# Performance work log

Hardware: AMD Instinct MI355X
Metric: run time of the kernel (lower is better)

Reference implementation:

```python
import jax, jax.numpy as jnp
import numpy as np

EMBED_DIM = 1024
NUM_HEADS = 16
HEAD_DIM = EMBED_DIM // NUM_HEADS
VOCAB = 5          # languages
BOTTLENECK = 800
SCALING = HEAD_DIM ** -0.5


def setup_inputs() -> dict:
    key = jax.random.key(0)
    ks = jax.random.split(key, 16)
    T, B, D = 2048, 2, EMBED_DIM
    s = 0.02
    return {
        "query": jax.random.normal(ks[0], (T, B, D), jnp.float32),
        "key": jax.random.normal(ks[1], (T, B, D), jnp.float32),
        "value": jax.random.normal(ks[2], (T, B, D), jnp.float32),
        "wq": jax.random.normal(ks[3], (D, D), jnp.float32) * s,
        "bq": jnp.zeros((D,), jnp.float32),
        "wk": jax.random.normal(ks[4], (D, D), jnp.float32) * s,
        "bk": jnp.zeros((D,), jnp.float32),
        "wv": jax.random.normal(ks[5], (D, D), jnp.float32) * s,
        "bv": jnp.zeros((D,), jnp.float32),
        "wo": jax.random.normal(ks[6], (D, D), jnp.float32) * s,
        "bo": jnp.zeros((D,), jnp.float32),
        "wte": jax.random.normal(ks[7], (VOCAB, D), jnp.float32) * s,
        "ct_w1": jax.random.normal(ks[8], (VOCAB, BOTTLENECK, D), jnp.float32) * s,
        "ct_b1": jnp.zeros((VOCAB, BOTTLENECK), jnp.float32),
        "ct_w2": jax.random.normal(ks[9], (VOCAB, 2 * D, BOTTLENECK), jnp.float32) * s,
        "ct_b2": jnp.zeros((VOCAB, 2 * D), jnp.float32),
        "language_id": jax.random.randint(ks[10], (B,), 0, VOCAB, jnp.int32),
    }


def _prefix_kv(language_id, wte, ct_w1, ct_b1, ct_w2, ct_b2):
    # PrefixTuningLangEmbLangspec: embed lang id, run all 5 bottleneck MLPs,
    # select per-sample MLP output via one-hot weighting, split into K/V.
    B = language_id.shape[0]
    emb = wte[language_id]                                  # [B, D]
    h = jnp.tanh(jnp.einsum("bd,chd->cbh", emb, ct_w1) + ct_b1[:, None, :])  # [5,B,800]
    kv = jnp.einsum("cbh,cdh->cbd", h, ct_w2) + ct_b2[:, None, :]            # [5,B,2D]
    w = jax.nn.one_hot(language_id, VOCAB, dtype=kv.dtype)  # [B,5]
    kv_sel = jnp.einsum("bc,cbd->bd", w, kv)                # [B,2D]
    # view(b,1,2,nh,hd): first D -> keys, second D -> values
    pk = kv_sel[:, :EMBED_DIM].reshape(B, NUM_HEADS, 1, HEAD_DIM)
    pv = kv_sel[:, EMBED_DIM:].reshape(B, NUM_HEADS, 1, HEAD_DIM)
    return pk, pv


def reference(query, key, value, wq, bq, wk, bk, wv, bv, wo, bo,
              wte, ct_w1, ct_b1, ct_w2, ct_b2, language_id):
    T, B, D = query.shape
    pk, pv = _prefix_kv(language_id, wte, ct_w1, ct_b1, ct_w2, ct_b2)  # [B,H,1,hd]

    # separate Q/K/V projections (Linear: x @ W^T + b)
    q = (jnp.einsum("tbd,ed->tbe", query, wq) + bq) * SCALING
    k = jnp.einsum("tbd,ed->tbe", key, wk) + bk
    v = jnp.einsum("tbd,ed->tbe", value, wv) + bv

    # [T,B,D] -> [B,H,T,hd]
    def split_heads(x):
        return x.reshape(T, B, NUM_HEADS, HEAD_DIM).transpose(1, 2, 0, 3)

    qh = split_heads(q)
    kh = jnp.concatenate([pk, split_heads(k)], axis=2)  # [B,H,T+1,hd]
    vh = jnp.concatenate([pv, split_heads(v)], axis=2)

    scores = jnp.einsum("bhqd,bhkd->bhqk", qh, kh)      # [B,H,T,T+1]
    attn = jax.nn.softmax(scores, axis=-1)
    ctx = jnp.einsum("bhqk,bhkd->bhqd", attn, vh)       # [B,H,T,hd]

    ctx = ctx.transpose(2, 0, 1, 3).reshape(T, B, D)    # back to [T,B,D]
    out = jnp.einsum("tbd,ed->tbe", ctx, wo) + bo
    return out
```

## Files before the change

kernel.cpp:

```cpp
#include <hip/hip_runtime.h>
#include <stdint.h>

#define T_SEQ 2048
#define BATCH 2
#define DIM   1024
#define NH    16
#define HD    64
#define TKP   2112

typedef _Float16 v8h __attribute__((ext_vector_type(8)));
typedef _Float16 v4h __attribute__((ext_vector_type(4)));
typedef __fp16   pkh2 __attribute__((ext_vector_type(2)));
typedef float    f32x4 __attribute__((ext_vector_type(4)));
typedef float    f32x16 __attribute__((ext_vector_type(16)));

__device__ __forceinline__ void gload16(const _Float16* g, _Float16* l) {
  __builtin_amdgcn_global_load_lds(
      (__attribute__((address_space(1))) unsigned int*)g,
      (__attribute__((address_space(3))) unsigned int*)l, 16, 0, 0);
}

__global__ void cvt_all(const float4* __restrict__ s0, const float4* __restrict__ s1,
                        const float4* __restrict__ s2, const float4* __restrict__ s3,
                        const float4* __restrict__ s4, const float4* __restrict__ s5,
                        const float4* __restrict__ s6,
                        v4h* __restrict__ d0, v4h* __restrict__ d1, v4h* __restrict__ d2,
                        v4h* __restrict__ d3, v4h* __restrict__ d4, v4h* __restrict__ d5,
                        v4h* __restrict__ d6) {
  const int NTB4 = 1048576, DD4 = 262144;
  int i = blockIdx.x * 256 + threadIdx.x;
  const float4* s; v4h* d; int off;
  if (i < 3 * NTB4) {
    int t = i / NTB4; off = i - t * NTB4;
    s = t == 0 ? s0 : t == 1 ? s1 : s2;
    d = t == 0 ? d0 : t == 1 ? d1 : d2;
  } else {
    int j = i - 3 * NTB4;
    int t = j / DD4; off = j - t * DD4;
    s = t == 0 ? s3 : t == 1 ? s4 : t == 2 ? s5 : s6;
    d = t == 0 ? d3 : t == 1 ? d4 : t == 2 ? d5 : d6;
  }
  float4 v = s[off];
  v4h o = { (_Float16)v.x, (_Float16)v.y, (_Float16)v.z, (_Float16)v.w };
  d[off] = o;
}

__global__ void prefix_pad_k(const float* __restrict__ wte, const float* __restrict__ w1,
                             const float* __restrict__ b1, const int* __restrict__ lang,
                             float* __restrict__ hbuf,
                             _Float16* __restrict__ kb, _Float16* __restrict__ vb) {
  if (blockIdx.x >= 400) {
    int bh = blockIdx.x - 400;
    v8h z = {};
    _Float16* kp = kb + ((size_t)bh * TKP + 2048) * 64;
    for (int i = threadIdx.x; i < 512; i += 256) *(v8h*)&kp[i * 8] = z;
    for (int i = threadIdx.x; i < 512; i += 256) {
      int c = i >> 3, seg = i & 7;
      *(v8h*)&vb[((size_t)bh * 64 + c) * TKP + 2048 + seg * 8] = z;
    }
    return;
  }
  int wid = blockIdx.x * 4 + (threadIdx.x >> 6);
  int lane = threadIdx.x & 63;
  int b = wid / 800, j = wid - b * 800;
  int c = lang[b];
  const float* wr = w1 + ((size_t)c * 800 + j) * 1024;
  const float* em = wte + (size_t)c * 1024;
  float s = 0.f;
  for (int d = lane; d < 1024; d += 64) s += wr[d] * em[d];
  for (int off = 32; off > 0; off >>= 1) s += __shfl_down(s, off, 64);
  if (lane == 0) hbuf[wid] = tanhf(s + b1[c * 800 + j]);
}

__global__ void prefix_kv_k(const float* __restrict__ w2, const float* __restrict__ b2,
                            const float* __restrict__ hbuf, const int* __restrict__ lang,
                            _Float16* __restrict__ kb, _Float16* __restrict__ vb) {
  int wid = blockIdx.x * 4 + (threadIdx.x >> 6);
  int lane = threadIdx.x & 63;
  int b = wid >> 11, e = wid & 2047;
  int c = lang[b];
  const float* wr = w2 + ((size_t)c * 2048 + e) * 800;
  const float* hb = hbuf + b * 800;
  float s = 0.f;
  for (int j = lane; j < 800; j += 64) s += wr[j] * hb[j];
  for (int off = 32; off > 0; off >>= 1) s += __shfl_down(s, off, 64);
  if (lane == 0) {
    float val = s + b2[c * 2048 + e];
    if (e < 1024) {
      int h = e >> 6, hd = e & 63;
      kb[((size_t)(b * 16 + h) * TKP + 2048) * 64 + hd] = (_Float16)val;
    } else {
      int d = e - 1024;
      int h = d >> 6, hd = d & 63;
      vb[((size_t)(b * 16 + h) * 64 + hd) * TKP + 2048] = (_Float16)val;
    }
  }
}

__global__ __launch_bounds__(256) void gemm_bt_k(
    const _Float16* __restrict__ A0, const _Float16* __restrict__ A1, const _Float16* __restrict__ A2,
    const _Float16* __restrict__ W0, const _Float16* __restrict__ W1, const _Float16* __restrict__ W2,
    const float* __restrict__ bs0, const float* __restrict__ bs1, const float* __restrict__ bs2,
    _Float16* __restrict__ qb, _Float16* __restrict__ kb, _Float16* __restrict__ vb,
    float* __restrict__ fout, int mode_base)
{
  __shared__ __align__(16) _Float16 smem[2][128 * 64 * 2];
  const int mode = mode_base + blockIdx.z;
  const _Float16* A = (mode == 1) ? A1 : (mode == 2) ? A2 : A0;
  const _Float16* W = (mode == 1) ? W1 : (mode == 2) ? W2 : W0;
  const float* bias = (mode == 1) ? bs1 : (mode == 2) ? bs2 : bs0;
  const int tid = threadIdx.x, w = tid >> 6, lane = tid & 63;
  const int quad = lane >> 4, l15 = lane & 15;
  const int r0 = blockIdx.x * 128, c0 = blockIdx.y * 128;
  const int wm = w >> 1, wn = w & 1;
  const int srow = lane >> 3, sseg = lane & 7;
  const int sw_seg = sseg ^ srow;
  const int rsw = l15 & 7;
  f32x4 acc[4][4] = {};

  auto stage = [&](int k0, int p) {
    _Float16* As = smem[p];
    _Float16* Bs = smem[p] + 8192;
#pragma unroll
    for (int i = 0; i < 4; ++i) {
      int rowb = w * 32 + i * 8;
      gload16(A + (size_t)(r0 + rowb + srow) * 1024 + k0 + sw_seg * 8, &As[rowb * 64]);
      gload16(W + (size_t)(c0 + rowb + srow) * 1024 + k0 + sw_seg * 8, &Bs[rowb * 64]);
    }
  };

  stage(0, 0);
  for (int t = 0; t < 16; ++t) {
    if (t < 15) {
      stage((t + 1) << 6, (t + 1) & 1);
      asm volatile("s_waitcnt vmcnt(8)" ::: "memory");
    } else {
      asm volatile("s_waitcnt vmcnt(0)" ::: "memory");
    }
    __builtin_amdgcn_s_barrier();
    __builtin_amdgcn_sched_barrier(0);
    const _Float16* As = smem[t & 1];
    const _Float16* Bs = smem[t & 1] + 8192;
#pragma unroll
    for (int ks = 0; ks < 2; ++ks) {
      v8h af[4], bfr[4];
#pragma unroll
      for (int mt = 0; mt < 4; ++mt)
        af[mt] = *(const v8h*)&As[(wm * 64 + mt * 16 + l15) * 64 + (((ks * 4 + quad) ^ rsw) * 8)];
#pragma unroll
      for (int nt = 0; nt < 4; ++nt)
        bfr[nt] = *(const v8h*)&Bs[(wn * 64 + nt * 16 + l15) * 64 + (((ks * 4 + quad) ^ rsw) * 8)];
#pragma unroll
      for (int mt = 0; mt < 4; ++mt)
#pragma unroll
        for (int nt = 0; nt < 4; ++nt)
          acc[mt][nt] = __builtin_amdgcn_mfma_f32_16x16x32_f16(af[mt], bfr[nt], acc[mt][nt], 0, 0, 0);
    }
    __builtin_amdgcn_sched_barrier(0);
    __builtin_amdgcn_s_barrier();
  }
  if (mode == 3) {
    for (int nt = 0; nt < 4; ++nt) {
      int e = c0 + wn * 64 + nt * 16 + l15;
      float be = bias[e];
      for (int mt = 0; mt < 4; ++mt) {
        int rb = r0 + wm * 64 + mt * 16 + quad * 4;
        for (int reg = 0; reg < 4; ++reg)
          fout[(size_t)(rb + reg) * 1024 + e] = acc[mt][nt][reg] + be;
      }
    }
    return;
  }
  _Float16* st = &smem[0][0] + w * 4096;
  const float qscale = (mode == 0) ? 0.125f * 1.44269504088896341f : 1.0f;
  for (int p = 0; p < 2; ++p) {
    __syncthreads();
    for (int ntl = 0; ntl < 2; ++ntl) {
      int nt = p * 2 + ntl;
      int e = c0 + wn * 64 + nt * 16 + l15;
      float be = bias[e];
      for (int mt = 0; mt < 4; ++mt)
        for (int reg = 0; reg < 4; ++reg) {
          float val = (acc[mt][nt][reg] + be) * qscale;
          int rl = mt * 16 + quad * 4 + reg;
          if (mode != 2) st[rl * 40 + ntl * 16 + l15] = (_Float16)val;
          else st[(ntl * 16 + l15) * 72 + (rl & 1) * 32 + (rl >> 1)] = (_Float16)val;
        }
    }
    __syncthreads();
    if (mode != 2) {
      for (int it = 0; it < 4; ++it) {
        int chunk = it * 64 + lane;
        int rr = chunk >> 2, seg = chunk & 3;
        v8h val = *(const v8h*)&st[rr * 40 + seg * 8];
        int r = r0 + wm * 64 + rr, b = r & 1, t = r >> 1;
        int e0 = c0 + wn * 64 + p * 32 + seg * 8;
        int h = e0 >> 6, hd0 = e0 & 63;
        if (mode == 0) *(v8h*)&qb[((size_t)(b * 16 + h) * 2048 + t) * 64 + hd0] = val;
        else           *(v8h*)&kb[((size_t)(b * 16 + h) * TKP + t) * 64 + hd0] = val;
      }
    } else {
      for (int it = 0; it < 4; ++it) {
        int chunk = it * 64 + lane;
        int el = chunk >> 3, b = (chunk >> 2) & 1, qs = chunk & 3;
        v8h val = *(const v8h*)&st[el * 72 + b * 32 + qs * 8];
        int e = c0 + wn * 64 + p * 32 + el;
        int h = e >> 6, hd = e & 63;
        int t0 = ((r0 + wm * 64) >> 1) + qs * 8;
        *(v8h*)&vb[((size_t)(b * 16 + h) * 64 + hd) * TKP + t0] = val;
      }
    }
  }
}

__global__ __launch_bounds__(256) void attn_k(
    const _Float16* __restrict__ qb, const _Float16* __restrict__ kb,
    const _Float16* __restrict__ vb, _Float16* __restrict__ ctx)
{
  __shared__ __align__(16) _Float16 Ks[2][64 * 72];
  __shared__ __align__(16) _Float16 Vs[2][64 * 72];
  const int bh = blockIdx.x;
  const int qt0 = blockIdx.y * 128;
  const int tid = threadIdx.x, w = tid >> 6, lane = tid & 63;
  const int l31 = lane & 31, h8 = (lane >> 5) * 8;
  v8h qf[4];
#pragma unroll
  for (int t = 0; t < 4; ++t)
    qf[t] = *(const v8h*)(qb + ((size_t)bh * 2048 + qt0 + w * 32 + l31) * 64 + t * 16 + h8);
  const int sr = tid >> 3, sseg = tid & 7;
  const _Float16* kptr = kb + (size_t)bh * TKP * 64 + sr * 64 + sseg * 8;
  const _Float16* vptr = vb + (size_t)bh * 64 * TKP + (size_t)sr * TKP + sseg * 8;
  int4 kp0 = *(const int4*)kptr, kp1 = *(const int4*)(kptr + 2048);
  int4 vp0 = *(const int4*)vptr, vp1 = *(const int4*)(vptr + 32 * TKP);
  kptr += 4096; vptr += 64;
  const int vcb = (sseg >> 1) * 32 + (sseg & 1) * 8;
  const v8h vones = { (_Float16)1.f, (_Float16)1.f, (_Float16)1.f, (_Float16)1.f,
                      (_Float16)1.f, (_Float16)1.f, (_Float16)1.f, (_Float16)1.f };
  f32x16 O0 = {}, O1 = {}, lacc = {};
  for (int kc = 0; kc < 33; ++kc) {
    _Float16* Kb = Ks[kc & 1];
    _Float16* Vb = Vs[kc & 1];
    *(int4*)&Kb[sr * 72 + sseg * 8] = kp0;
    *(int4*)&Kb[(sr + 32) * 72 + sseg * 8] = kp1;
    {
      char* vr0 = (char*)&Vb[sr * 72];
      char* vr1 = (char*)&Vb[(sr + 32) * 72];
      *(int2*)(vr0 + vcb)      = *(int2*)&vp0;
      *(int2*)(vr0 + vcb + 16) = *((int2*)&vp0 + 1);
      *(int2*)(vr1 + vcb)      = *(int2*)&vp1;
      *(int2*)(vr1 + vcb + 16) = *((int2*)&vp1 + 1);
    }
    __syncthreads();
    if (kc < 32) {
      kp0 = *(const int4*)kptr; kp1 = *(const int4*)(kptr + 2048);
      vp0 = *(const int4*)vptr; vp1 = *(const int4*)(vptr + 32 * TKP);
      kptr += 4096; vptr += 64;
    }
    f32x16 S0 = {}, S1 = {};
    __builtin_amdgcn_s_setprio(1);
#pragma unroll
    for (int t = 0; t < 4; ++t) {
      v8h kf0 = *(const v8h*)&Kb[(l31) * 72 + t * 16 + h8];
      v8h kf1 = *(const v8h*)&Kb[(32 + l31) * 72 + t * 16 + h8];
      S0 = __builtin_amdgcn_mfma_f32_32x32x16_f16(kf0, qf[t], S0, 0, 0, 0);
      S1 = __builtin_amdgcn_mfma_f32_32x32x16_f16(kf1, qf[t], S1, 0, 0, 0);
    }
    __builtin_amdgcn_s_setprio(0);
    if (kc == 32) {
#pragma unroll
      for (int r = 0; r < 16; ++r) {
        if (r > 0) S0[r] = -1e30f;
        S1[r] = -1e30f;
      }
      if (lane >= 32) S0[0] = -1e30f;
    }
    __builtin_amdgcn_s_setprio(1);
#pragma unroll
    for (int c = 0; c < 4; ++c) {
      union { v8h v; pkh2 p[4]; } f;
      if (c == 0) {
        f.p[0] = __builtin_amdgcn_cvt_pkrtz(__builtin_amdgcn_exp2f(S0[0]), __builtin_amdgcn_exp2f(S0[1]));
        f.p[1] = __builtin_amdgcn_cvt_pkrtz(__builtin_amdgcn_exp2f(S0[2]), __builtin_amdgcn_exp2f(S0[3]));
        f.p[2] = __builtin_amdgcn_cvt_pkrtz(__builtin_amdgcn_exp2f(S0[4]), __builtin_amdgcn_exp2f(S0[5]));
        f.p[3] = __builtin_amdgcn_cvt_pkrtz(__builtin_amdgcn_exp2f(S0[6]), __builtin_amdgcn_exp2f(S0[7]));
      } else if (c == 1) {
        f.p[0] = __builtin_amdgcn_cvt_pkrtz(__builtin_amdgcn_exp2f(S0[8]),  __builtin_amdgcn_exp2f(S0[9]));
        f.p[1] = __builtin_amdgcn_cvt_pkrtz(__builtin_amdgcn_exp2f(S0[10]), __builtin_amdgcn_exp2f(S0[11]));
        f.p[2] = __builtin_amdgcn_cvt_pkrtz(__builtin_amdgcn_exp2f(S0[12]), __builtin_amdgcn_exp2f(S0[13]));
        f.p[3] = __builtin_amdgcn_cvt_pkrtz(__builtin_amdgcn_exp2f(S0[14]), __builtin_amdgcn_exp2f(S0[15]));
      } else if (c == 2) {
        f.p[0] = __builtin_amdgcn_cvt_pkrtz(__builtin_amdgcn_exp2f(S1[0]), __builtin_amdgcn_exp2f(S1[1]));
        f.p[1] = __builtin_amdgcn_cvt_pkrtz(__builtin_amdgcn_exp2f(S1[2]), __builtin_amdgcn_exp2f(S1[3]));
        f.p[2] = __builtin_amdgcn_cvt_pkrtz(__builtin_amdgcn_exp2f(S1[4]), __builtin_amdgcn_exp2f(S1[5]));
        f.p[3] = __builtin_amdgcn_cvt_pkrtz(__builtin_amdgcn_exp2f(S1[6]), __builtin_amdgcn_exp2f(S1[7]));
      } else {
        f.p[0] = __builtin_amdgcn_cvt_pkrtz(__builtin_amdgcn_exp2f(S1[8]),  __builtin_amdgcn_exp2f(S1[9]));
        f.p[1] = __builtin_amdgcn_cvt_pkrtz(__builtin_amdgcn_exp2f(S1[10]), __builtin_amdgcn_exp2f(S1[11]));
        f.p[2] = __builtin_amdgcn_cvt_pkrtz(__builtin_amdgcn_exp2f(S1[12]), __builtin_amdgcn_exp2f(S1[13]));
        f.p[3] = __builtin_amdgcn_cvt_pkrtz(__builtin_amdgcn_exp2f(S1[14]), __builtin_amdgcn_exp2f(S1[15]));
      }
      v8h vf0 = *(const v8h*)&Vb[(l31) * 72 + c * 16 + h8];
      v8h vf1 = *(const v8h*)&Vb[(32 + l31) * 72 + c * 16 + h8];
      O0 = __builtin_amdgcn_mfma_f32_32x32x16_f16(vf0, f.v, O0, 0, 0, 0);
      O1 = __builtin_amdgcn_mfma_f32_32x32x16_f16(vf1, f.v, O1, 0, 0, 0);
      lacc = __builtin_amdgcn_mfma_f32_32x32x16_f16(vones, f.v, lacc, 0, 0, 0);
    }
    __builtin_amdgcn_s_setprio(0);
  }
  const float inv = 1.f / lacc[0];
  const int b = bh >> 4, hh = bh & 15;
  const int q = qt0 + w * 32 + l31;
  _Float16* cbase = ctx + ((size_t)q * 2 + b) * 1024 + hh * 64 + (h8 >> 1);
#pragma unroll
  for (int rq = 0; rq < 4; ++rq) {
    v4h o0 = { (_Float16)(O0[rq * 4 + 0] * inv), (_Float16)(O0[rq * 4 + 1] * inv),
               (_Float16)(O0[rq * 4 + 2] * inv), (_Float16)(O0[rq * 4 + 3] * inv) };
    *(v4h*)(cbase + rq * 8) = o0;
    v4h o1 = { (_Float16)(O1[rq * 4 + 0] * inv), (_Float16)(O1[rq * 4 + 1] * inv),
               (_Float16)(O1[rq * 4 + 2] * inv), (_Float16)(O1[rq * 4 + 3] * inv) };
    *(v4h*)(cbase + 32 + rq * 8) = o1;
  }
}

extern "C" void kernel_launch(void* const* d_in, const int* in_sizes, int n_in,
                              void* d_out, int out_size, void* d_ws, size_t ws_size,
                              hipStream_t stream) {
  (void)in_sizes; (void)n_in; (void)out_size; (void)ws_size;
  const float* query = (const float*)d_in[0];
  const float* key_  = (const float*)d_in[1];
  const float* value = (const float*)d_in[2];
  const float* wq = (const float*)d_in[3];
  const float* bq = (const float*)d_in[4];
  const float* wk = (const float*)d_in[5];
  const float* bk = (const float*)d_in[6];
  const float* wv = (const float*)d_in[7];
  const float* bv = (const float*)d_in[8];
  const float* wo = (const float*)d_in[9];
  const float* bo = (const float*)d_in[10];
  const float* wte = (const float*)d_in[11];
  const float* w1 = (const float*)d_in[12];
  const float* b1 = (const float*)d_in[13];
  const float* w2 = (const float*)d_in[14];
  const float* b2 = (const float*)d_in[15];
  const int* lang = (const int*)d_in[16];
  float* out = (float*)d_out;

  const size_t NTB = (size_t)T_SEQ * BATCH * DIM;
  const size_t DD  = (size_t)DIM * DIM;
  const size_t KVN = (size_t)BATCH * NH * TKP * HD;
  _Float16* xq  = (_Float16*)d_ws;
  _Float16* xk  = xq + NTB;
  _Float16* xv  = xk + NTB;
  _Float16* wqb = xv + NTB;
  _Float16* wkb = wqb + DD;
  _Float16* wvb = wkb + DD;
  _Float16* wob = wvb + DD;
  _Float16* qbuf = wob + DD;
  _Float16* kbuf = qbuf + NTB;
  _Float16* vbuf = kbuf + KVN;
  float* hbuf = (float*)(vbuf + KVN);
  _Float16* ctxb = xq;

  cvt_all<<<16384, 256, 0, stream>>>((const float4*)query, (const float4*)key_,
                                     (const float4*)value, (const float4*)wq,
                                     (const float4*)wk, (const float4*)wv, (const float4*)wo,
                                     (v4h*)xq, (v4h*)xk, (v4h*)xv, (v4h*)wqb,
                                     (v4h*)wkb, (v4h*)wvb, (v4h*)wob);
  prefix_pad_k<<<432, 256, 0, stream>>>(wte, w1, b1, lang, hbuf, kbuf, vbuf);
  prefix_kv_k<<<1024, 256, 0, stream>>>(w2, b2, hbuf, lang, kbuf, vbuf);
  gemm_bt_k<<<dim3(32, 8, 3), 256, 0, stream>>>(xq, xk, xv, wqb, wkb, wvb, bq, bk, bv,
                                                qbuf, kbuf, vbuf, nullptr, 0);
  attn_k<<<dim3(32, 16), 256, 0, stream>>>(qbuf, kbuf, vbuf, ctxb);
  gemm_bt_k<<<dim3(32, 8, 1), 256, 0, stream>>>(ctxb, ctxb, ctxb, wob, wob, wob, bo, bo, bo,
                                                qbuf, kbuf, vbuf, out, 3);
}
```

Before: 273.0 us.

## Double attention key tile to 128 and peel final prefix/mask tile

```diff
diff --git a/kernel.cpp b/kernel.cpp
--- a/kernel.cpp
+++ b/kernel.cpp
@@ -213,12 +213,12 @@
   }
 }
 
-__global__ __launch_bounds__(256) void attn_k(
+__global__ __launch_bounds__(256, 1) void attn_k(
     const _Float16* __restrict__ qb, const _Float16* __restrict__ kb,
     const _Float16* __restrict__ vb, _Float16* __restrict__ ctx)
 {
-  __shared__ __align__(16) _Float16 Ks[2][64 * 72];
-  __shared__ __align__(16) _Float16 Vs[2][64 * 72];
+  __shared__ __align__(16) _Float16 Ks[2][128 * 72];
+  __shared__ __align__(16) _Float16 Vs[2][64 * 136];
   const int bh = blockIdx.x;
   const int qt0 = blockIdx.y * 128;
   const int tid = threadIdx.x, w = tid >> 6, lane = tid & 63;
@@ -230,32 +230,91 @@
   const int sr = tid >> 3, sseg = tid & 7;
   const _Float16* kptr = kb + (size_t)bh * TKP * 64 + sr * 64 + sseg * 8;
   const _Float16* vptr = vb + (size_t)bh * 64 * TKP + (size_t)sr * TKP + sseg * 8;
-  int4 kp0 = *(const int4*)kptr, kp1 = *(const int4*)(kptr + 2048);
-  int4 vp0 = *(const int4*)vptr, vp1 = *(const int4*)(vptr + 32 * TKP);
-  kptr += 4096; vptr += 64;
   const int vcb = (sseg >> 1) * 32 + (sseg & 1) * 8;
+  int4 kp[4], vp[4];
+#pragma unroll
+  for (int j = 0; j < 4; ++j) kp[j] = *(const int4*)(kptr + j * 2048);
+#pragma unroll
+  for (int j = 0; j < 2; ++j)
+#pragma unroll
+    for (int g = 0; g < 2; ++g)
+      vp[j * 2 + g] = *(const int4*)(vptr + (size_t)j * 32 * TKP + g * 64);
+  kptr += 8192; vptr += 128;
   const v8h vones = { (_Float16)1.f, (_Float16)1.f, (_Float16)1.f, (_Float16)1.f,
                       (_Float16)1.f, (_Float16)1.f, (_Float16)1.f, (_Float16)1.f };
   f32x16 O0 = {}, O1 = {}, lacc = {};
-  for (int kc = 0; kc < 33; ++kc) {
+  for (int kc = 0; kc < 16; ++kc) {
     _Float16* Kb = Ks[kc & 1];
     _Float16* Vb = Vs[kc & 1];
-    *(int4*)&Kb[sr * 72 + sseg * 8] = kp0;
-    *(int4*)&Kb[(sr + 32) * 72 + sseg * 8] = kp1;
-    {
-      char* vr0 = (char*)&Vb[sr * 72];
-      char* vr1 = (char*)&Vb[(sr + 32) * 72];
-      *(int2*)(vr0 + vcb)      = *(int2*)&vp0;
-      *(int2*)(vr0 + vcb + 16) = *((int2*)&vp0 + 1);
-      *(int2*)(vr1 + vcb)      = *(int2*)&vp1;
-      *(int2*)(vr1 + vcb + 16) = *((int2*)&vp1 + 1);
-    }
+#pragma unroll
+    for (int j = 0; j < 4; ++j)
+      *(int4*)&Kb[(sr + 32 * j) * 72 + sseg * 8] = kp[j];
+#pragma unroll
+    for (int j = 0; j < 2; ++j)
+#pragma unroll
+      for (int g = 0; g < 2; ++g) {
+        char* vr = (char*)&Vb[(sr + 32 * j) * 136] + g * 128 + vcb;
+        *(int2*)(vr)      = *(int2*)&vp[j * 2 + g];
+        *(int2*)(vr + 16) = *((int2*)&vp[j * 2 + g] + 1);
+      }
     __syncthreads();
-    if (kc < 32) {
-      kp0 = *(const int4*)kptr; kp1 = *(const int4*)(kptr + 2048);
-      vp0 = *(const int4*)vptr; vp1 = *(const int4*)(vptr + 32 * TKP);
-      kptr += 4096; vptr += 64;
-    }
+    if (kc < 15) {
+#pragma unroll
+      for (int j = 0; j < 4; ++j) kp[j] = *(const int4*)(kptr + j * 2048);
+#pragma unroll
+      for (int j = 0; j < 2; ++j)
+#pragma unroll
+        for (int g = 0; g < 2; ++g)
+          vp[j * 2 + g] = *(const int4*)(vptr + (size_t)j * 32 * TKP + g * 64);
+      kptr += 8192; vptr += 128;
+    } else {
+      kp[0] = *(const int4*)kptr;
+      kp[1] = *(const int4*)(kptr + 2048);
+      vp[0] = *(const int4*)vptr;
+      vp[1] = *(const int4*)(vptr + (size_t)32 * TKP);
+    }
+    f32x16 S[4] = { {}, {}, {}, {} };
+    __builtin_amdgcn_s_setprio(1);
+#pragma unroll
+    for (int t = 0; t < 4; ++t) {
+#pragma unroll
+      for (int j = 0; j < 4; ++j) {
+        v8h kf = *(const v8h*)&Kb[(32 * j + l31) * 72 + t * 16 + h8];
+        S[j] = __builtin_amdgcn_mfma_f32_32x32x16_f16(kf, qf[t], S[j], 0, 0, 0);
+      }
+    }
+#pragma unroll
+    for (int c = 0; c < 8; ++c) {
+      const int b0 = (c & 1) * 8;
+      union { v8h v; pkh2 p[4]; } f;
+      f.p[0] = __builtin_amdgcn_cvt_pkrtz(__builtin_amdgcn_exp2f(S[c >> 1][b0 + 0]),
+                                          __builtin_amdgcn_exp2f(S[c >> 1][b0 + 1]));
+      f.p[1] = __builtin_amdgcn_cvt_pkrtz(__builtin_amdgcn_exp2f(S[c >> 1][b0 + 2]),
+                                          __builtin_amdgcn_exp2f(S[c >> 1][b0 + 3]));
+      f.p[2] = __builtin_amdgcn_cvt_pkrtz(__builtin_amdgcn_exp2f(S[c >> 1][b0 + 4]),
+                                          __builtin_amdgcn_exp2f(S[c >> 1][b0 + 5]));
+      f.p[3] = __builtin_amdgcn_cvt_pkrtz(__builtin_amdgcn_exp2f(S[c >> 1][b0 + 6]),
+                                          __builtin_amdgcn_exp2f(S[c >> 1][b0 + 7]));
+      v8h vf0 = *(const v8h*)&Vb[(l31) * 136 + c * 16 + h8];
+      v8h vf1 = *(const v8h*)&Vb[(32 + l31) * 136 + c * 16 + h8];
+      O0 = __builtin_amdgcn_mfma_f32_32x32x16_f16(vf0, f.v, O0, 0, 0, 0);
+      O1 = __builtin_amdgcn_mfma_f32_32x32x16_f16(vf1, f.v, O1, 0, 0, 0);
+      lacc = __builtin_amdgcn_mfma_f32_32x32x16_f16(vones, f.v, lacc, 0, 0, 0);
+    }
+    __builtin_amdgcn_s_setprio(0);
+  }
+  {
+    _Float16* Kb = Ks[0];
+    _Float16* Vb = Vs[0];
+    *(int4*)&Kb[sr * 72 + sseg * 8] = kp[0];
+    *(int4*)&Kb[(sr + 32) * 72 + sseg * 8] = kp[1];
+#pragma unroll
+    for (int j = 0; j < 2; ++j) {
+      char* vr = (char*)&Vb[(sr + 32 * j) * 136] + vcb;
+      *(int2*)(vr)      = *(int2*)&vp[j];
+      *(int2*)(vr + 16) = *((int2*)&vp[j] + 1);
+    }
+    __syncthreads();
     f32x16 S0 = {}, S1 = {};
     __builtin_amdgcn_s_setprio(1);
 #pragma unroll
@@ -266,41 +325,28 @@
       S1 = __builtin_amdgcn_mfma_f32_32x32x16_f16(kf1, qf[t], S1, 0, 0, 0);
     }
     __builtin_amdgcn_s_setprio(0);
-    if (kc == 32) {
-#pragma unroll
-      for (int r = 0; r < 16; ++r) {
-        if (r > 0) S0[r] = -1e30f;
-        S1[r] = -1e30f;
-      }
-      if (lane >= 32) S0[0] = -1e30f;
-    }
+#pragma unroll
+    for (int r = 0; r < 16; ++r) {
+      if (r > 0) S0[r] = -1e30f;
+      S1[r] = -1e30f;
+    }
+    if (lane >= 32) S0[0] = -1e30f;
     __builtin_amdgcn_s_setprio(1);
 #pragma unroll
     for (int c = 0; c < 4; ++c) {
+      const int b0 = (c & 1) * 8;
       union { v8h v; pkh2 p[4]; } f;
-      if (c == 0) {
-        f.p[0] = __builtin_amdgcn_cvt_pkrtz(__builtin_amdgcn_exp2f(S0[0]), __builtin_amdgcn_exp2f(S0[1]));
-        f.p[1] = __builtin_amdgcn_cvt_pkrtz(__builtin_amdgcn_exp2f(S0[2]), __builtin_amdgcn_exp2f(S0[3]));
-        f.p[2] = __builtin_amdgcn_cvt_pkrtz(__builtin_amdgcn_exp2f(S0[4]), __builtin_amdgcn_exp2f(S0[5]));
-        f.p[3] = __builtin_amdgcn_cvt_pkrtz(__builtin_amdgcn_exp2f(S0[6]), __builtin_amdgcn_exp2f(S0[7]));
-      } else if (c == 1) {
-        f.p[0] = __builtin_amdgcn_cvt_pkrtz(__builtin_amdgcn_exp2f(S0[8]),  __builtin_amdgcn_exp2f(S0[9]));
-        f.p[1] = __builtin_amdgcn_cvt_pkrtz(__builtin_amdgcn_exp2f(S0[10]), __builtin_amdgcn_exp2f(S0[11]));
-        f.p[2] = __builtin_amdgcn_cvt_pkrtz(__builtin_amdgcn_exp2f(S0[12]), __builtin_amdgcn_exp2f(S0[13]));
-        f.p[3] = __builtin_amdgcn_cvt_pkrtz(__builtin_amdgcn_exp2f(S0[14]), __builtin_amdgcn_exp2f(S0[15]));
-      } else if (c == 2) {
-        f.p[0] = __builtin_amdgcn_cvt_pkrtz(__builtin_amdgcn_exp2f(S1[0]), __builtin_amdgcn_exp2f(S1[1]));
-        f.p[1] = __builtin_amdgcn_cvt_pkrtz(__builtin_amdgcn_exp2f(S1[2]), __builtin_amdgcn_exp2f(S1[3]));
-        f.p[2] = __builtin_amdgcn_cvt_pkrtz(__builtin_amdgcn_exp2f(S1[4]), __builtin_amdgcn_exp2f(S1[5]));
-        f.p[3] = __builtin_amdgcn_cvt_pkrtz(__builtin_amdgcn_exp2f(S1[6]), __builtin_amdgcn_exp2f(S1[7]));
-      } else {
-        f.p[0] = __builtin_amdgcn_cvt_pkrtz(__builtin_amdgcn_exp2f(S1[8]),  __builtin_amdgcn_exp2f(S1[9]));
-        f.p[1] = __builtin_amdgcn_cvt_pkrtz(__builtin_amdgcn_exp2f(S1[10]), __builtin_amdgcn_exp2f(S1[11]));
-        f.p[2] = __builtin_amdgcn_cvt_pkrtz(__builtin_amdgcn_exp2f(S1[12]), __builtin_amdgcn_exp2f(S1[13]));
-        f.p[3] = __builtin_amdgcn_cvt_pkrtz(__builtin_amdgcn_exp2f(S1[14]), __builtin_amdgcn_exp2f(S1[15]));
-      }
-      v8h vf0 = *(const v8h*)&Vb[(l31) * 72 + c * 16 + h8];
-      v8h vf1 = *(const v8h*)&Vb[(32 + l31) * 72 + c * 16 + h8];
+      const f32x16& Sx = (c < 2) ? S0 : S1;
+      f.p[0] = __builtin_amdgcn_cvt_pkrtz(__builtin_amdgcn_exp2f(Sx[b0 + 0]),
+                                          __builtin_amdgcn_exp2f(Sx[b0 + 1]));
+      f.p[1] = __builtin_amdgcn_cvt_pkrtz(__builtin_amdgcn_exp2f(Sx[b0 + 2]),
+                                          __builtin_amdgcn_exp2f(Sx[b0 + 3]));
+      f.p[2] = __builtin_amdgcn_cvt_pkrtz(__builtin_amdgcn_exp2f(Sx[b0 + 4]),
+                                          __builtin_amdgcn_exp2f(Sx[b0 + 5]));
+      f.p[3] = __builtin_amdgcn_cvt_pkrtz(__builtin_amdgcn_exp2f(Sx[b0 + 6]),
+                                          __builtin_amdgcn_exp2f(Sx[b0 + 7]));
+      v8h vf0 = *(const v8h*)&Vb[(l31) * 136 + c * 16 + h8];
+      v8h vf1 = *(const v8h*)&Vb[(32 + l31) * 136 + c * 16 + h8];
       O0 = __builtin_amdgcn_mfma_f32_32x32x16_f16(vf0, f.v, O0, 0, 0, 0);
       O1 = __builtin_amdgcn_mfma_f32_32x32x16_f16(vf1, f.v, O1, 0, 0, 0);
       lacc = __builtin_amdgcn_mfma_f32_32x32x16_f16(vones, f.v, lacc, 0, 0, 0);
```

After: 287.4 us. 5.3% more time.
